# Optimization experiments

Hardware: AMD Instinct MI355X
Metric: run time of the kernel (lower is better)

The kernel has to match this reference:

```python
import jax, jax.numpy as jnp
import numpy as np

B = 256      # graph pairs
NPG = 28     # nodes per graph
MAXN = 32    # max_node_set_size
EPG = 64     # edges per graph (== max_edge_set_size, so no edge padding)
MAXE = 64
D = 128      # node_state_dim
FN = 32      # raw node feature dim
FE = 32      # raw edge feature dim
SK = 64      # sinkhorn_feature_dim
STEPS = 3    # propagation_steps
TEMP = 0.1
ITERS = 20
CW = 0.9     # consistency_weight
G = 2 * B
N = G * NPG
E = G * EPG


def _lin(key, fi, fo):
    return jax.random.normal(key, (fi, fo), jnp.float32) / np.sqrt(fi)


def setup_inputs() -> dict:
    key = jax.random.key(0)
    ks = jax.random.split(key, 12)
    rng = np.random.default_rng(0)
    off = (np.arange(G) * NPG)[:, None]   # graphs ordered q0,c0,q1,c1,...
    from_idx = jnp.asarray((rng.integers(0, NPG, (G, EPG)) + off).reshape(-1), jnp.int32)
    to_idx = jnp.asarray((rng.integers(0, NPG, (G, EPG)) + off).reshape(-1), jnp.int32)
    return dict(
        node_features=jax.random.normal(ks[0], (N, FN), jnp.float32),
        edge_features=jax.random.normal(ks[1], (E, FE), jnp.float32),
        enc_nw=_lin(ks[2], FN, D), enc_nb=jnp.zeros((D,), jnp.float32),
        enc_ew=_lin(ks[3], FE, D), enc_eb=jnp.zeros((D,), jnp.float32),
        msg_w1=_lin(ks[4], 3 * D, 2 * D), msg_b1=jnp.zeros((2 * D,), jnp.float32),
        msg_w2=_lin(ks[5], 2 * D, D), msg_b2=jnp.zeros((D,), jnp.float32),
        rmsg_w1=_lin(ks[6], 3 * D, 2 * D), rmsg_b1=jnp.zeros((2 * D,), jnp.float32),
        rmsg_w2=_lin(ks[7], 2 * D, D), rmsg_b2=jnp.zeros((D,), jnp.float32),
        upd_w1=_lin(ks[8], 2 * D, 2 * D), upd_b1=jnp.zeros((2 * D,), jnp.float32),
        upd_w2=_lin(ks[9], 2 * D, D), upd_b2=jnp.zeros((D,), jnp.float32),
        sk_w1=_lin(ks[10], D, SK), sk_b1=jnp.zeros((SK,), jnp.float32),
        sk_w2=_lin(ks[11], SK, SK), sk_b2=jnp.zeros((SK,), jnp.float32),
        from_idx=from_idx, to_idx=to_idx,
        query_sizes=jnp.full((B,), NPG, jnp.int32),
        corpus_sizes=jnp.full((B,), NPG, jnp.int32),
    )


def _mlp2(x, w1, b1, w2, b2):
    return jnp.maximum(x @ w1 + b1, 0.0) @ w2 + b2


def _sinkhorn(log_alpha):
    # log-domain sinkhorn (noise_factor = 0 -> deterministic)
    la = log_alpha / TEMP
    for _ in range(ITERS):
        la = la - jax.nn.logsumexp(la, axis=2, keepdims=True)
        la = la - jax.nn.logsumexp(la, axis=1, keepdims=True)
    return jnp.exp(la)


def _align(q, c, plan):
    # feature_alignment_score: -relu(q - P @ c).sum over set and feature dims
    return -jnp.maximum(q - plan @ c, 0.0).sum(axis=(1, 2))


def _forward(node_features, edge_features, enc_nw, enc_nb, enc_ew, enc_eb,
             msg_w1, msg_b1, msg_w2, msg_b2, rmsg_w1, rmsg_b1, rmsg_w2, rmsg_b2,
             upd_w1, upd_b1, upd_w2, upd_b2, sk_w1, sk_b1, sk_w2, sk_b2,
             from_idx, to_idx, query_sizes, corpus_sizes):
    h = node_features @ enc_nw + enc_nb        # encoder, [N, D]
    e = edge_features @ enc_ew + enc_eb        # [E, D]

    def messages(h):
        f = _mlp2(jnp.concatenate([h[from_idx], h[to_idx], e], -1), msg_w1, msg_b1, msg_w2, msg_b2)
        r = _mlp2(jnp.concatenate([h[to_idx], h[from_idx], e], -1), rmsg_w1, rmsg_b1, rmsg_w2, rmsg_b2)
        return f, r

    for _ in range(STEPS):  # GraphPropLayer x propagation_steps
        f, r = messages(h)
        agg = jax.ops.segment_sum(f, to_idx, num_segments=N) + \
              jax.ops.segment_sum(r, from_idx, num_segments=N)
        h = h + _mlp2(jnp.concatenate([agg, h], -1), upd_w1, upd_b1, upd_w2, upd_b2)

    # split_and_stack nodes: graphs alternate query/corpus, pad NPG -> MAXN
    hs = jnp.pad(h.reshape(B, 2, NPG, D), ((0, 0), (0, 0), (0, MAXN - NPG), (0, 0)))
    q_nodes, c_nodes = hs[:, 0], hs[:, 1]      # [B, MAXN, D]

    tq = _mlp2(q_nodes, sk_w1, sk_b1, sk_w2, sk_b2)
    tc = _mlp2(c_nodes, sk_w1, sk_b1, sk_w2, sk_b2)
    pos = jnp.arange(MAXN)[None, :]
    mq = tq * (pos < query_sizes[:, None])[..., None]
    mc = tc * (pos < corpus_sizes[:, None])[..., None]
    node_plan = _sinkhorn(jnp.einsum('bqd,bcd->bqc', mq, mc))   # [B, MAXN, MAXN]

    # propagation_messages on final node states
    f, r = messages(h)
    em = (f + r).reshape(B, 2, EPG, D)         # EPG == MAXE -> no pad
    q_edges, c_edges = em[:, 0], em[:, 1]

    # local (within-graph) endpoint indices for kronecker lookup
    fl = (from_idx % NPG).reshape(B, 2, EPG)
    tl = (to_idx % NPG).reshape(B, 2, EPG)
    qf, cf = fl[:, 0], fl[:, 1]
    qt, ct = tl[:, 0], tl[:, 1]

    def kron(T, qf, qt, cf, ct):
        straight = T[qf][:, cf] * T[qt][:, ct]   # [MAXE, MAXE]
        cross = T[qf][:, ct] * T[qt][:, cf]
        return straight + cross

    edge_scores = jax.vmap(kron)(node_plan, qf, qt, cf, ct)     # [B, MAXE, MAXE]
    edge_plan = _sinkhorn(edge_scores)

    return _align(q_nodes, c_nodes, node_plan) + CW * _align(q_edges, c_edges, edge_plan)


def reference(node_features, edge_features, enc_nw, enc_nb, enc_ew, enc_eb,
              msg_w1, msg_b1, msg_w2, msg_b2, rmsg_w1, rmsg_b1, rmsg_w2, rmsg_b2,
              upd_w1, upd_b1, upd_w2, upd_b2, sk_w1, sk_b1, sk_w2, sk_b2,
              from_idx, to_idx, query_sizes, corpus_sizes):
    return _forward(node_features, edge_features, enc_nw, enc_nb, enc_ew, enc_eb,
                    msg_w1, msg_b1, msg_w2, msg_b2, rmsg_w1, rmsg_b1, rmsg_w2, rmsg_b2,
                    upd_w1, upd_b1, upd_w2, upd_b2, sk_w1, sk_b1, sk_w2, sk_b2,
                    from_idx, to_idx, query_sizes, corpus_sizes)
```

## Files before the change

### kernel.cpp

```cpp
#include <hip/hip_runtime.h>
#include <math.h>

#define NPG 28
#define EPG 64
#define NB  256
#define NG  512
#define NN  14336
#define NE  32768
#define TEMPINV 10.0f
#define SINK_ITERS 20
#define CW 0.9f

typedef unsigned int uint;
typedef unsigned short ushort;
typedef __attribute__((ext_vector_type(8))) __bf16 bf16x8;
typedef __attribute__((ext_vector_type(4))) float f32x4;

__device__ __forceinline__ ushort f2bf(float x) {
    uint u = __float_as_uint(x);
    u += 0x7fffu + ((u >> 16) & 1u);
    return (ushort)(u >> 16);
}
__device__ __forceinline__ uint f2bf2(float lo, float hi) {
    return (uint)f2bf(lo) | ((uint)f2bf(hi) << 16);
}
__device__ __forceinline__ float bflo(uint w) { return __uint_as_float(w << 16); }
__device__ __forceinline__ float bfhi(uint w) { return __uint_as_float(w & 0xffff0000u); }
__device__ __forceinline__ uint relu_sum_pk(uint w1, uint w2, uint w3) {
    float lo = fmaxf(bflo(w1) + bflo(w2) + bflo(w3), 0.f);
    float hi = fmaxf(bfhi(w1) + bfhi(w2) + bfhi(w3), 0.f);
    return f2bf2(lo, hi);
}
__device__ __forceinline__ f32x4 mfma16(bf16x8 a, bf16x8 b, f32x4 c) {
    return __builtin_amdgcn_mfma_f32_16x16x32_bf16(a, b, c, 0, 0, 0);
}

__global__ __launch_bounds__(512, 4) void gnn_fused(
    float* __restrict__ h,
    const ushort* __restrict__ EC2,
    const ushort* __restrict__ WhpL,
    const ushort* __restrict__ W2fL, const ushort* __restrict__ W2rL,
    const float* __restrict__ b2f, const float* __restrict__ b2r,
    const ushort* __restrict__ UW1T, const float* __restrict__ ub1,
    const ushort* __restrict__ UW2T, const float* __restrict__ ub2,
    const int* __restrict__ from_idx, const int* __restrict__ to_idx,
    float* __restrict__ EM)
{
    __shared__ ushort HPs[NPG * 520];
    __shared__ float acc_s[NPG * 132];
    __shared__ float hs[NPG * 132];
    __shared__ int fl[64], tl[64];
    const int g = blockIdx.x;
    const int tid = threadIdx.x;
    const int w = tid >> 6, lane = tid & 63;
    const int li = lane & 15, quad = lane >> 4;
    const int wm = w >> 1, wn = w & 1;
    ushort* hid = &HPs[0];

    if (tid < 64) {
        fl[tid] = from_idx[g * 64 + tid] - g * NPG;
        tl[tid] = to_idx[g * 64 + tid] - g * NPG;
    }
    for (int u = tid; u < NPG * 128; u += 512)
        hs[(u >> 7) * 132 + (u & 127)] = h[(size_t)g * (NPG * 128) + u];
    __syncthreads();

#pragma unroll 1
    for (int step = 0; step < 3; ++step) {
        uint4 ha[2][4];
#pragma unroll
        for (int mi = 0; mi < 2; ++mi) {
            const int row = mi * 16 + li;
            const int rr = (row < NPG) ? row : 0;
#pragma unroll
            for (int kb = 0; kb < 4; ++kb) {
                const float* src = &hs[rr * 132 + kb * 32 + quad * 8];
                const float4 f0 = *(const float4*)src;
                const float4 f1 = *(const float4*)(src + 4);
                uint4 o;
                o.x = f2bf2(f0.x, f0.y);
                o.y = f2bf2(f0.z, f0.w);
                o.z = f2bf2(f1.x, f1.y);
                o.w = f2bf2(f1.z, f1.w);
                ha[mi][kb] = o;
            }
        }
        for (int u = tid; u < NPG * 132; u += 512) acc_s[u] = 0.f;

        f32x4 acc[4];
#pragma unroll
        for (int j = 0; j < 4; ++j) acc[j] = f32x4{0.f, 0.f, 0.f, 0.f};

#pragma unroll 1
        for (int p = 0; p < 2; ++p) {
            {
                const int colw = w * 64;
#pragma unroll
                for (int ni = 0; ni < 4; ++ni) {
                    const int col = colw + ni * 16 + li;
                    const ushort* pb = WhpL + (size_t)(p * 512 + col) * 32 + quad * 8;
                    f32x4 c0 = f32x4{0.f, 0.f, 0.f, 0.f};
                    f32x4 c1 = f32x4{0.f, 0.f, 0.f, 0.f};
#pragma unroll
                    for (int kb = 0; kb < 4; ++kb) {
                        const bf16x8 b = __builtin_bit_cast(bf16x8,
                            *(const uint4*)(pb + (size_t)kb * 32768));
                        c0 = mfma16(__builtin_bit_cast(bf16x8, ha[0][kb]), b, c0);
                        c1 = mfma16(__builtin_bit_cast(bf16x8, ha[1][kb]), b, c1);
                    }
#pragma unroll
                    for (int r = 0; r < 4; ++r) {
                        const int r0 = quad * 4 + r;
                        HPs[r0 * 520 + col] = f2bf(c0[r]);
                        const int r1 = 16 + quad * 4 + r;
                        if (r1 < NPG) HPs[r1 * 520 + col] = f2bf(c1[r]);
                    }
                }
            }
            __syncthreads();
            if (p == 1) {
#pragma unroll
                for (int j = 0; j < 4; ++j) acc[j] = f32x4{0.f, 0.f, 0.f, 0.f};
            }
            const int e = wm * 16 + li;
            const int i1 = p ? tl[e] : fl[e];
            const int i2 = p ? fl[e] : tl[e];
            const int ad1 = i1 * 520 + quad * 8;
            const int ad2 = i2 * 520 + 256 + quad * 8;
            const int ade = e * 32 + quad * 8;
            const ushort* ecb = EC2 + (size_t)(g * 2 + p) * 16384;
            const ushort* W2L = p ? W2rL : W2fL;
            const int n0 = wn * 64;
            const ushort* pb[4];
#pragma unroll
            for (int ni = 0; ni < 4; ++ni)
                pb[ni] = W2L + (size_t)(n0 + ni * 16 + li) * 32 + quad * 8;
#pragma unroll
            for (int kb = 0; kb < 8; ++kb) {
                const uint4 u1 = *(const uint4*)&HPs[ad1 + kb * 32];
                const uint4 u2 = *(const uint4*)&HPs[ad2 + kb * 32];
                const uint4 ue = *(const uint4*)(ecb + kb * 2048 + ade);
                uint4 o;
                o.x = relu_sum_pk(u1.x, u2.x, ue.x);
                o.y = relu_sum_pk(u1.y, u2.y, ue.y);
                o.z = relu_sum_pk(u1.z, u2.z, ue.z);
                o.w = relu_sum_pk(u1.w, u2.w, ue.w);
                const bf16x8 a = __builtin_bit_cast(bf16x8, o);
#pragma unroll
                for (int ni = 0; ni < 4; ++ni) {
                    const bf16x8 b = __builtin_bit_cast(bf16x8,
                        *(const uint4*)(pb[ni] + (size_t)kb * 4096));
                    acc[ni] = mfma16(a, b, acc[ni]);
                }
            }
            {
                const int* targ = p ? fl : tl;
                const float* bias = p ? b2r : b2f;
                float bv[4];
#pragma unroll
                for (int ni = 0; ni < 4; ++ni) bv[ni] = bias[n0 + ni * 16 + li];
#pragma unroll
                for (int r = 0; r < 4; ++r) {
                    const int loc = targ[wm * 16 + quad * 4 + r];
#pragma unroll
                    for (int ni = 0; ni < 4; ++ni)
                        atomicAdd(&acc_s[loc * 132 + n0 + ni * 16 + li],
                                  acc[ni][r] + bv[ni]);
                }
            }
            __syncthreads();
        }

        {
            const int n0u = w * 32;
            f32x4 ua[2][2];
#pragma unroll
            for (int mi = 0; mi < 2; ++mi)
#pragma unroll
                for (int ni = 0; ni < 2; ++ni) ua[mi][ni] = f32x4{0.f, 0.f, 0.f, 0.f};
            const ushort* pb0 = UW1T + (size_t)(n0u + li) * 256 + quad * 8;
            const ushort* pb1 = UW1T + (size_t)(n0u + 16 + li) * 256 + quad * 8;
#pragma unroll
            for (int kb = 0; kb < 8; ++kb) {
                bf16x8 a[2];
                if (kb < 4) {
#pragma unroll
                    for (int mi = 0; mi < 2; ++mi) {
                        const int row = mi * 16 + li;
                        const int rr = (row < NPG) ? row : 0;
                        const float* src = &acc_s[rr * 132 + kb * 32 + quad * 8];
                        const float4 f0 = *(const float4*)src;
                        const float4 f1 = *(const float4*)(src + 4);
                        uint4 o;
                        o.x = f2bf2(f0.x, f0.y);
                        o.y = f2bf2(f0.z, f0.w);
                        o.z = f2bf2(f1.x, f1.y);
                        o.w = f2bf2(f1.z, f1.w);
                        a[mi] = __builtin_bit_cast(bf16x8, o);
                    }
                } else {
                    a[0] = __builtin_bit_cast(bf16x8, ha[0][kb - 4]);
                    a[1] = __builtin_bit_cast(bf16x8, ha[1][kb - 4]);
                }
                const bf16x8 b0 = __builtin_bit_cast(bf16x8, *(const uint4*)(pb0 + kb * 32));
                const bf16x8 b1 = __builtin_bit_cast(bf16x8, *(const uint4*)(pb1 + kb * 32));
#pragma unroll
                for (int mi = 0; mi < 2; ++mi) {
                    ua[mi][0] = mfma16(a[mi], b0, ua[mi][0]);
                    ua[mi][1] = mfma16(a[mi], b1, ua[mi][1]);
                }
            }
            const float bv0 = ub1[n0u + li], bv1 = ub1[n0u + 16 + li];
#pragma unroll
            for (int mi = 0; mi < 2; ++mi)
#pragma unroll
                for (int r = 0; r < 4; ++r) {
                    const int row = mi * 16 + quad * 4 + r;
                    if (row < NPG) {
                        hid[row * 264 + n0u + li] = f2bf(fmaxf(ua[mi][0][r] + bv0, 0.f));
                        hid[row * 264 + n0u + 16 + li] = f2bf(fmaxf(ua[mi][1][r] + bv1, 0.f));
                    }
                }
        }
        __syncthreads();
        {
            const int n0u = w * 16;
            f32x4 ua[2];
            ua[0] = f32x4{0.f, 0.f, 0.f, 0.f};
            ua[1] = f32x4{0.f, 0.f, 0.f, 0.f};
            const ushort* pb0 = UW2T + (size_t)(n0u + li) * 256 + quad * 8;
#pragma unroll
            for (int kb = 0; kb < 8; ++kb) {
                bf16x8 a[2];
#pragma unroll
                for (int mi = 0; mi < 2; ++mi) {
                    const int row = mi * 16 + li;
                    const int rr = (row < NPG) ? row : 0;
                    a[mi] = __builtin_bit_cast(bf16x8,
                        *(const uint4*)&hid[rr * 264 + kb * 32 + quad * 8]);
                }
                const bf16x8 b0 = __builtin_bit_cast(bf16x8, *(const uint4*)(pb0 + kb * 32));
                ua[0] = mfma16(a[0], b0, ua[0]);
                ua[1] = mfma16(a[1], b0, ua[1]);
            }
            const float bv = ub2[n0u + li];
#pragma unroll
            for (int mi = 0; mi < 2; ++mi)
#pragma unroll
                for (int r = 0; r < 4; ++r) {
                    const int row = mi * 16 + quad * 4 + r;
                    if (row < NPG)
                        hs[row * 132 + n0u + li] += ua[mi][r] + bv;
                }
        }
        __syncthreads();
    }

    {
        uint4 ha[2][4];
#pragma unroll
        for (int mi = 0; mi < 2; ++mi) {
            const int row = mi * 16 + li;
            const int rr = (row < NPG) ? row : 0;
#pragma unroll
            for (int kb = 0; kb < 4; ++kb) {
                const float* src = &hs[rr * 132 + kb * 32 + quad * 8];
                const float4 f0 = *(const float4*)src;
                const float4 f1 = *(const float4*)(src + 4);
                uint4 o;
                o.x = f2bf2(f0.x, f0.y);
                o.y = f2bf2(f0.z, f0.w);
                o.z = f2bf2(f1.x, f1.y);
                o.w = f2bf2(f1.z, f1.w);
                ha[mi][kb] = o;
            }
        }
        f32x4 acc[4];
#pragma unroll
        for (int j = 0; j < 4; ++j) acc[j] = f32x4{0.f, 0.f, 0.f, 0.f};
        const int n0 = wn * 64;
#pragma unroll 1
        for (int p = 0; p < 2; ++p) {
            {
                const int colw = w * 64;
#pragma unroll
                for (int ni = 0; ni < 4; ++ni) {
                    const int col = colw + ni * 16 + li;
                    const ushort* pb = WhpL + (size_t)(p * 512 + col) * 32 + quad * 8;
                    f32x4 c0 = f32x4{0.f, 0.f, 0.f, 0.f};
                    f32x4 c1 = f32x4{0.f, 0.f, 0.f, 0.f};
#pragma unroll
                    for (int kb = 0; kb < 4; ++kb) {
                        const bf16x8 b = __builtin_bit_cast(bf16x8,
                            *(const uint4*)(pb + (size_t)kb * 32768));
                        c0 = mfma16(__builtin_bit_cast(bf16x8, ha[0][kb]), b, c0);
                        c1 = mfma16(__builtin_bit_cast(bf16x8, ha[1][kb]), b, c1);
                    }
#pragma unroll
                    for (int r = 0; r < 4; ++r) {
                        const int r0 = quad * 4 + r;
                        HPs[r0 * 520 + col] = f2bf(c0[r]);
                        const int r1 = 16 + quad * 4 + r;
                        if (r1 < NPG) HPs[r1 * 520 + col] = f2bf(c1[r]);
                    }
                }
            }
            __syncthreads();
            const int e = wm * 16 + li;
            const int i1 = p ? tl[e] : fl[e];
            const int i2 = p ? fl[e] : tl[e];
            const int ad1 = i1 * 520 + quad * 8;
            const int ad2 = i2 * 520 + 256 + quad * 8;
            const int ade = e * 32 + quad * 8;
            const ushort* ecb = EC2 + (size_t)(g * 2 + p) * 16384;
            const ushort* W2L = p ? W2rL : W2fL;
            const ushort* pb[4];
#pragma unroll
            for (int ni = 0; ni < 4; ++ni)
                pb[ni] = W2L + (size_t)(n0 + ni * 16 + li) * 32 + quad * 8;
#pragma unroll
            for (int kb = 0; kb < 8; ++kb) {
                const uint4 u1 = *(const uint4*)&HPs[ad1 + kb * 32];
                const uint4 u2 = *(const uint4*)&HPs[ad2 + kb * 32];
                const uint4 ue = *(const uint4*)(ecb + kb * 2048 + ade);
                uint4 o;
                o.x = relu_sum_pk(u1.x, u2.x, ue.x);
                o.y = relu_sum_pk(u1.y, u2.y, ue.y);
                o.z = relu_sum_pk(u1.z, u2.z, ue.z);
                o.w = relu_sum_pk(u1.w, u2.w, ue.w);
                const bf16x8 a = __builtin_bit_cast(bf16x8, o);
#pragma unroll
                for (int ni = 0; ni < 4; ++ni) {
                    const bf16x8 b = __builtin_bit_cast(bf16x8,
                        *(const uint4*)(pb[ni] + (size_t)kb * 4096));
                    acc[ni] = mfma16(a, b, acc[ni]);
                }
            }
            __syncthreads();
        }
        float bv[4];
#pragma unroll
        for (int ni = 0; ni < 4; ++ni)
            bv[ni] = b2f[n0 + ni * 16 + li] + b2r[n0 + ni * 16 + li];
#pragma unroll
        for (int r = 0; r < 4; ++r) {
            const int erow = g * 64 + wm * 16 + quad * 4 + r;
#pragma unroll
            for (int ni = 0; ni < 4; ++ni)
                EM[(size_t)erow * 128 + n0 + ni * 16 + li] = acc[ni][r] + bv[ni];
        }
    }
    for (int u = tid; u < NPG * 128; u += 512)
        h[(size_t)g * (NPG * 128) + u] = hs[(u >> 7) * 132 + (u & 127)];
}

template<int TM, bool OUTBF, bool OUT2, bool ECL>
__global__ __launch_bounds__(256) void gemm2(
    const float* __restrict__ A, int lda, int K,
    const float* __restrict__ W, int ldw, const float* __restrict__ bias,
    float* __restrict__ C, ushort* __restrict__ Cb, int ldc)
{
    constexpr int BM = TM * 16;
    constexpr int AV = BM / 64;
    __shared__ float As[16][BM + 4];
    __shared__ float Bs[16][132];
    const int tid = threadIdx.x;
    const int m0 = blockIdx.x * BM;
    const int n0 = blockIdx.y * 128;
    const int tx = tid & 15, ty = tid >> 4;
    const int arow = (AV == 2) ? (tid >> 1) : (tid >> 2);
    const int a0   = (AV == 2) ? ((tid & 1) * 8) : ((tid & 3) * 4);
    const int brow = ty;
    const int bcol = tx * 8;
    const int nch = K >> 4;

    float4 aC[2], bC[2], aN[2], bN[2];
    float acc[TM][8];
#pragma unroll
    for (int i = 0; i < TM; ++i)
#pragma unroll
        for (int j = 0; j < 8; ++j) acc[i][j] = 0.f;

    {
        const float* src = A + (size_t)(m0 + arow) * lda + a0;
        aC[0] = *(const float4*)src;
        if (AV == 2) aC[1] = *(const float4*)(src + 4);
        const float* bsrc = W + (size_t)brow * ldw + n0 + bcol;
        bC[0] = *(const float4*)bsrc;
        bC[1] = *(const float4*)(bsrc + 4);
    }

    for (int ch = 0; ch < nch; ++ch) {
        {
            const float* f = (const float*)aC;
#pragma unroll
            for (int i = 0; i < AV * 4; ++i) As[a0 + i][arow] = f[i];
            *(float4*)&Bs[brow][bcol]     = bC[0];
            *(float4*)&Bs[brow][bcol + 4] = bC[1];
        }
        __syncthreads();
        if (ch + 1 < nch) {
            const int kc = (ch + 1) << 4;
            const float* src = A + (size_t)(m0 + arow) * lda + kc + a0;
            aN[0] = *(const float4*)src;
            if (AV == 2) aN[1] = *(const float4*)(src + 4);
            const float* bsrc = W + (size_t)(kc + brow) * ldw + n0 + bcol;
            bN[0] = *(const float4*)bsrc;
            bN[1] = *(const float4*)(bsrc + 4);
        }
#pragma unroll
        for (int kk = 0; kk < 16; ++kk) {
            float afr[TM], bfr[8];
#pragma unroll
            for (int i = 0; i < TM; i += 4)
                *(float4*)&afr[i] = *(const float4*)&As[kk][ty * TM + i];
            *(float4*)&bfr[0] = *(const float4*)&Bs[kk][tx * 8];
            *(float4*)&bfr[4] = *(const float4*)&Bs[kk][tx * 8 + 4];
#pragma unroll
            for (int i = 0; i < TM; ++i)
#pragma unroll
                for (int j = 0; j < 8; ++j) acc[i][j] = fmaf(afr[i], bfr[j], acc[i][j]);
        }
        __syncthreads();
        aC[0] = aN[0]; aC[1] = aN[1];
        bC[0] = bN[0]; bC[1] = bN[1];
    }
#pragma unroll
    for (int i = 0; i < TM; ++i) {
        const int row = m0 + ty * TM + i;
#pragma unroll
        for (int j = 0; j < 8; ++j) {
            const int col = n0 + tx * 8 + j;
            float v = acc[i][j] + bias[col];
            if (ECL) {
                const int gg = row >> 6, eloc = row & 63;
                const int p = col >> 8, kb = (col >> 5) & 7, jj = col & 31;
                Cb[(size_t)(((gg * 2 + p) * 8 + kb)) * 2048 + eloc * 32 + jj] = f2bf(v);
            } else if (OUTBF) {
                Cb[(size_t)row * ldc + col] = f2bf(v);
            } else {
                C[(size_t)row * ldc + col] = v;
                if (OUT2) Cb[(size_t)row * ldc + col] = f2bf(v);
            }
        }
    }
}

__global__ __launch_bounds__(256) void pack2(
    const float* __restrict__ msg_w1, const float* __restrict__ rmsg_w1,
    const float* __restrict__ msg_b1, const float* __restrict__ rmsg_b1,
    const float* __restrict__ enc_ew, const float* __restrict__ enc_eb,
    const float* __restrict__ msg_w2, const float* __restrict__ rmsg_w2,
    const float* __restrict__ upd_w1, const float* __restrict__ upd_w2,
    float* __restrict__ Wcomb, float* __restrict__ bcomb,
    ushort* __restrict__ WhpL, ushort* __restrict__ W2fL, ushort* __restrict__ W2rL,
    ushort* __restrict__ UW1T, ushort* __restrict__ UW2T)
{
    const int gid = blockIdx.x, tid = threadIdx.x;
    if (gid < 64) {
        const int idx = gid * 256 + tid;
        const int a = idx >> 9, n = idx & 511;
        const float* Wsrc = (n < 256) ? msg_w1 : rmsg_w1;
        const int nc = n & 255;
        float s = 0.f;
        for (int j = 0; j < 128; ++j)
            s = fmaf(enc_ew[a * 128 + j], Wsrc[(256 + j) * 256 + nc], s);
        Wcomb[idx] = s;
    } else if (gid < 66) {
        const int n = (gid - 64) * 256 + tid;
        const float* Wsrc = (n < 256) ? msg_w1 : rmsg_w1;
        const float* bsrc = (n < 256) ? msg_b1 : rmsg_b1;
        const int nc = n & 255;
        float s = bsrc[nc];
        for (int j = 0; j < 128; ++j)
            s = fmaf(enc_eb[j], Wsrc[(256 + j) * 256 + nc], s);
        bcomb[n] = s;
    } else if (gid < 578) {
        const int idx = (gid - 66) * 256 + tid;
        const int n = idx >> 7, k = idx & 127;
        const float* Wsrc = (n < 512) ? msg_w1 : rmsg_w1;
        const int part = (n >> 8) & 1, col = n & 255;
        WhpL[(size_t)(k >> 5) * 32768 + n * 32 + (k & 31)] =
            f2bf(Wsrc[(part * 128 + k) * 256 + col]);
    } else if (gid < 706) {
        const int idx = (gid - 578) * 256 + tid;
        const int n = idx >> 8, k = idx & 255;
        W2fL[(size_t)(k >> 5) * 4096 + n * 32 + (k & 31)] = f2bf(msg_w2[k * 128 + n]);
    } else if (gid < 834) {
        const int idx = (gid - 706) * 256 + tid;
        const int n = idx >> 8, k = idx & 255;
        W2rL[(size_t)(k >> 5) * 4096 + n * 32 + (k & 31)] = f2bf(rmsg_w2[k * 128 + n]);
    } else if (gid < 1090) {
        const int idx = (gid - 834) * 256 + tid;
        const int n = idx >> 8, k = idx & 255;
        UW1T[idx] = f2bf(upd_w1[k * 256 + n]);
    } else {
        const int idx = (gid - 1090) * 256 + tid;
        const int n = idx >> 8, k = idx & 255;
        UW2T[idx] = f2bf(upd_w2[k * 128 + n]);
    }
}

__global__ __launch_bounds__(256) void node_kernel(
    const float* __restrict__ h,
    const float* __restrict__ w1, const float* __restrict__ b1,
    const float* __restrict__ w2, const float* __restrict__ b2,
    const int* __restrict__ qsz, const int* __restrict__ csz,
    float* __restrict__ plan_out, float* __restrict__ loss_out)
{
    __shared__ float qn[32][128];
    __shared__ float cn[32][128];
    __shared__ float t1[32][64];
    __shared__ float mq[32][68];
    __shared__ float mc[32][68];
    __shared__ float la[32][33];
    __shared__ float red[4];
    const int bb = blockIdx.x;
    const int tid = threadIdx.x;
    const int qs = qsz[bb], cs = csz[bb];
    for (int u = tid * 4; u < 4096; u += 1024) {
        const int p = u >> 7, d = u & 127;
        float4 zq = make_float4(0.f, 0.f, 0.f, 0.f), zc = zq;
        if (p < NPG) {
            zq = *(const float4*)(h + (size_t)((2 * bb) * NPG + p) * 128 + d);
            zc = *(const float4*)(h + (size_t)((2 * bb + 1) * NPG + p) * 128 + d);
        }
        *(float4*)&qn[p][d] = zq;
        *(float4*)&cn[p][d] = zc;
    }
    __syncthreads();
    const int col = tid & 63;
    const int rg  = tid >> 6;
    for (int s = 0; s < 2; ++s) {
        const float (*src)[128] = s ? cn : qn;
        float (*dst)[68] = s ? mc : mq;
        const int sz = s ? cs : qs;
        float a8[8];
#pragma unroll
        for (int u = 0; u < 8; ++u) a8[u] = b1[col];
        for (int k = 0; k < 128; ++k) {
            const float wv = w1[k * 64 + col];
#pragma unroll
            for (int u = 0; u < 8; ++u) a8[u] = fmaf(src[rg + 4 * u][k], wv, a8[u]);
        }
#pragma unroll
        for (int u = 0; u < 8; ++u) t1[rg + 4 * u][col] = fmaxf(a8[u], 0.f);
        __syncthreads();
#pragma unroll
        for (int u = 0; u < 8; ++u) a8[u] = b2[col];
        for (int k = 0; k < 64; ++k) {
            const float wv = w2[k * 64 + col];
#pragma unroll
            for (int u = 0; u < 8; ++u) a8[u] = fmaf(t1[rg + 4 * u][k], wv, a8[u]);
        }
#pragma unroll
        for (int u = 0; u < 8; ++u) {
            const int r = rg + 4 * u;
            dst[r][col] = (r < sz) ? a8[u] : 0.f;
        }
        __syncthreads();
    }
    {
        const int q = tid >> 3, cg = tid & 7;
#pragma unroll
        for (int u = 0; u < 4; ++u) {
            const int c = cg + 8 * u;
            float s = 0.f;
            for (int d = 0; d < 64; ++d) s = fmaf(mq[q][d], mc[c][d], s);
            la[q][c] = s * TEMPINV;
        }
    }
    __syncthreads();
    const int l8 = tid & 7, rq = tid >> 3;
    for (int it = 0; it < SINK_ITERS; ++it) {
        {
            float x[4];
#pragma unroll
            for (int u = 0; u < 4; ++u) x[u] = la[rq][l8 * 4 + u];
            float m = fmaxf(fmaxf(x[0], x[1]), fmaxf(x[2], x[3]));
            m = fmaxf(m, __shfl_xor(m, 1));
            m = fmaxf(m, __shfl_xor(m, 2));
            m = fmaxf(m, __shfl_xor(m, 4));
            float s = __expf(x[0] - m) + __expf(x[1] - m) + __expf(x[2] - m) + __expf(x[3] - m);
            s += __shfl_xor(s, 1);
            s += __shfl_xor(s, 2);
            s += __shfl_xor(s, 4);
            const float lse = m + __logf(s);
#pragma unroll
            for (int u = 0; u < 4; ++u) la[rq][l8 * 4 + u] = x[u] - lse;
        }
        __syncthreads();
        {
            float x[4];
#pragma unroll
            for (int u = 0; u < 4; ++u) x[u] = la[l8 * 4 + u][rq];
            float m = fmaxf(fmaxf(x[0], x[1]), fmaxf(x[2], x[3]));
            m = fmaxf(m, __shfl_xor(m, 1));
            m = fmaxf(m, __shfl_xor(m, 2));
            m = fmaxf(m, __shfl_xor(m, 4));
            float s = __expf(x[0] - m) + __expf(x[1] - m) + __expf(x[2] - m) + __expf(x[3] - m);
            s += __shfl_xor(s, 1);
            s += __shfl_xor(s, 2);
            s += __shfl_xor(s, 4);
            const float lse = m + __logf(s);
#pragma unroll
            for (int u = 0; u < 4; ++u) la[l8 * 4 + u][rq] = x[u] - lse;
        }
        __syncthreads();
    }
    for (int u = tid; u < 1024; u += 256) {
        const int q = u >> 5, c = u & 31;
        const float p = __expf(la[q][c]);
        la[q][c] = p;
        plan_out[(size_t)bb * 1024 + u] = p;
    }
    __syncthreads();
    float lsum = 0.f;
    {
        const int q = tid >> 3, dg = tid & 7;
        for (int u = 0; u < 16; ++u) {
            const int d = dg + 8 * u;
            float pc = 0.f;
#pragma unroll
            for (int c = 0; c < 32; ++c) pc = fmaf(la[q][c], cn[c][d], pc);
            lsum += fmaxf(qn[q][d] - pc, 0.f);
        }
    }
#pragma unroll
    for (int off = 1; off < 64; off <<= 1) lsum += __shfl_xor(lsum, off);
    if ((tid & 63) == 0) red[tid >> 6] = lsum;
    __syncthreads();
    if (tid == 0) loss_out[bb] = -(red[0] + red[1] + red[2] + red[3]);
}

__global__ __launch_bounds__(256) void edge_kernel(
    const float* __restrict__ plan, const float* __restrict__ EM,
    const int* __restrict__ from_idx, const int* __restrict__ to_idx,
    float* __restrict__ loss_out)
{
    __shared__ float T[32][33];
    __shared__ float la[64][65];
    __shared__ float ce[64][128];
    __shared__ int qf[64], qt[64], cfi[64], cti[64];
    __shared__ float red[4];
    const int bb = blockIdx.x;
    const int tid = threadIdx.x;
    for (int u = tid; u < 1024; u += 256) T[u >> 5][u & 31] = plan[(size_t)bb * 1024 + u];
    if (tid < 64) {
        const int gq = 2 * bb, gc = 2 * bb + 1;
        qf[tid]  = from_idx[gq * 64 + tid] - gq * NPG;
        qt[tid]  = to_idx  [gq * 64 + tid] - gq * NPG;
        cfi[tid] = from_idx[gc * 64 + tid] - gc * NPG;
        cti[tid] = to_idx  [gc * 64 + tid] - gc * NPG;
    }
    {
        const int gc = 2 * bb + 1;
        for (int u = tid * 4; u < 8192; u += 1024) {
            const int i = u >> 7, d = u & 127;
            *(float4*)&ce[i][d] = *(const float4*)(EM + (size_t)(gc * 64 + i) * 128 + d);
        }
    }
    __syncthreads();
    {
        const int i = tid >> 2, jg = tid & 3;
        const int a = qf[i], b_ = qt[i];
#pragma unroll
        for (int u = 0; u < 16; ++u) {
            const int j = jg * 16 + u;
            const float s = T[a][cfi[j]] * T[b_][cti[j]] + T[a][cti[j]] * T[b_][cfi[j]];
            la[i][j] = s * TEMPINV;
        }
    }
    __syncthreads();
    const int l4 = tid & 3, rr = tid >> 2;
    for (int it = 0; it < SINK_ITERS; ++it) {
        {
            float x[16];
#pragma unroll
            for (int u = 0; u < 16; ++u) x[u] = la[rr][l4 * 16 + u];
            float m = x[0];
#pragma unroll
            for (int u = 1; u < 16; ++u) m = fmaxf(m, x[u]);
            m = fmaxf(m, __shfl_xor(m, 1));
            m = fmaxf(m, __shfl_xor(m, 2));
            float s = 0.f;
#pragma unroll
            for (int u = 0; u < 16; ++u) s += __expf(x[u] - m);
            s += __shfl_xor(s, 1);
            s += __shfl_xor(s, 2);
            const float lse = m + __logf(s);
#pragma unroll
            for (int u = 0; u < 16; ++u) la[rr][l4 * 16 + u] = x[u] - lse;
        }
        __syncthreads();
        {
            float x[16];
#pragma unroll
            for (int u = 0; u < 16; ++u) x[u] = la[l4 * 16 + u][rr];
            float m = x[0];
#pragma unroll
            for (int u = 1; u < 16; ++u) m = fmaxf(m, x[u]);
            m = fmaxf(m, __shfl_xor(m, 1));
            m = fmaxf(m, __shfl_xor(m, 2));
            float s = 0.f;
#pragma unroll
            for (int u = 0; u < 16; ++u) s += __expf(x[u] - m);
            s += __shfl_xor(s, 1);
            s += __shfl_xor(s, 2);
            const float lse = m + __logf(s);
#pragma unroll
            for (int u = 0; u < 16; ++u) la[l4 * 16 + u][rr] = x[u] - lse;
        }
        __syncthreads();
    }
    for (int u = tid; u < 4096; u += 256) la[u >> 6][u & 63] = __expf(la[u >> 6][u & 63]);
    __syncthreads();
    float lsum = 0.f;
    {
        const int q = tid >> 2, dg = tid & 3;
        const float* qe = EM + (size_t)((2 * bb) * 64 + q) * 128;
        for (int u = 0; u < 32; ++u) {
            const int d = dg + 4 * u;
            float pc = 0.f;
            for (int c = 0; c < 64; ++c) pc = fmaf(la[q][c], ce[c][d], pc);
            lsum += fmaxf(qe[d] - pc, 0.f);
        }
    }
#pragma unroll
    for (int off = 1; off < 64; off <<= 1) lsum += __shfl_xor(lsum, off);
    if ((tid & 63) == 0) red[tid >> 6] = lsum;
    __syncthreads();
    if (tid == 0) loss_out[bb] -= CW * (red[0] + red[1] + red[2] + red[3]);
}

extern "C" void kernel_launch(void* const* d_in, const int* in_sizes, int n_in,
                              void* d_out, int out_size, void* d_ws, size_t ws_size,
                              hipStream_t stream)
{
    const float* node_features = (const float*)d_in[0];
    const float* edge_features = (const float*)d_in[1];
    const float* enc_nw  = (const float*)d_in[2];
    const float* enc_nb  = (const float*)d_in[3];
    const float* enc_ew  = (const float*)d_in[4];
    const float* enc_eb  = (const float*)d_in[5];
    const float* msg_w1  = (const float*)d_in[6];
    const float* msg_b1  = (const float*)d_in[7];
    const float* msg_w2  = (const float*)d_in[8];
    const float* msg_b2  = (const float*)d_in[9];
    const float* rmsg_w1 = (const float*)d_in[10];
    const float* rmsg_b1 = (const float*)d_in[11];
    const float* rmsg_w2 = (const float*)d_in[12];
    const float* rmsg_b2 = (const float*)d_in[13];
    const float* upd_w1  = (const float*)d_in[14];
    const float* upd_b1  = (const float*)d_in[15];
    const float* upd_w2  = (const float*)d_in[16];
    const float* upd_b2  = (const float*)d_in[17];
    const float* sk_w1   = (const float*)d_in[18];
    const float* sk_b1   = (const float*)d_in[19];
    const float* sk_w2   = (const float*)d_in[20];
    const float* sk_b2   = (const float*)d_in[21];
    const int* from_idx  = (const int*)d_in[22];
    const int* to_idx    = (const int*)d_in[23];
    const int* qsizes    = (const int*)d_in[24];
    const int* csizes    = (const int*)d_in[25];
    float* out = (float*)d_out;

    float* ws    = (float*)d_ws;
    float* h     = ws;
    float* EM    = h + (size_t)NN * 128;
    float* plan  = EM + (size_t)NE * 128;
    float* Wcomb = plan + (size_t)NB * 1024;
    float* bcomb = Wcomb + 16384;
    ushort* EC2  = (ushort*)(bcomb + 512);
    ushort* WhpL = EC2 + (size_t)NE * 512;
    ushort* W2fL = WhpL + 131072;
    ushort* W2rL = W2fL + 32768;
    ushort* UW1T = W2rL + 32768;
    ushort* UW2T = UW1T + 65536;

    const dim3 blk(256);
    const dim3 blk512(512);

    pack2<<<1218, blk, 0, stream>>>(msg_w1, rmsg_w1, msg_b1, rmsg_b1,
                                    enc_ew, enc_eb, msg_w2, rmsg_w2, upd_w1, upd_w2,
                                    Wcomb, bcomb, WhpL, W2fL, W2rL, UW1T, UW2T);
    gemm2<4, false, false, false><<<dim3(NN / 64, 1), blk, 0, stream>>>(
        node_features, 32, 32, enc_nw, 128, enc_nb, h, nullptr, 128);
    gemm2<8, false, false, true><<<dim3(NE / 128, 4), blk, 0, stream>>>(
        edge_features, 32, 32, Wcomb, 512, bcomb, nullptr, EC2, 512);

    gnn_fused<<<dim3(NG), blk512, 0, stream>>>(
        h, EC2, WhpL, W2fL, W2rL, msg_b2, rmsg_b2,
        UW1T, upd_b1, UW2T, upd_b2, from_idx, to_idx, EM);

    node_kernel<<<NB, blk, 0, stream>>>(
        h, sk_w1, sk_b1, sk_w2, sk_b2, qsizes, csizes, plan, out);
    edge_kernel<<<NB, blk, 0, stream>>>(
        plan, EM, from_idx, to_idx, out);
}
```

Measured before the change: 553.7 us.

## Process two graphs per block in fused GNN kernel to reuse weight fragments

```diff
diff --git a/kernel.cpp b/kernel.cpp
--- a/kernel.cpp
+++ b/kernel.cpp
@@ -35,7 +35,7 @@
     return __builtin_amdgcn_mfma_f32_16x16x32_bf16(a, b, c, 0, 0, 0);
 }
 
-__global__ __launch_bounds__(512, 4) void gnn_fused(
+__global__ __launch_bounds__(512, 2) void gnn_fused(
     float* __restrict__ h,
     const ushort* __restrict__ EC2,
     const ushort* __restrict__ WhpL,
@@ -46,50 +46,52 @@
     const int* __restrict__ from_idx, const int* __restrict__ to_idx,
     float* __restrict__ EM)
 {
-    __shared__ ushort HPs[NPG * 520];
-    __shared__ float acc_s[NPG * 132];
-    __shared__ float hs[NPG * 132];
-    __shared__ int fl[64], tl[64];
+    __shared__ ushort HPs[2][NPG * 520];
+    __shared__ float acc_s[2][NPG * 132];
+    __shared__ float hs[2][NPG * 132];
+    __shared__ int fl[2][64], tl[2][64];
     const int g = blockIdx.x;
     const int tid = threadIdx.x;
     const int w = tid >> 6, lane = tid & 63;
     const int li = lane & 15, quad = lane >> 4;
     const int wm = w >> 1, wn = w & 1;
-    ushort* hid = &HPs[0];
-
-    if (tid < 64) {
-        fl[tid] = from_idx[g * 64 + tid] - g * NPG;
-        tl[tid] = to_idx[g * 64 + tid] - g * NPG;
-    }
-    for (int u = tid; u < NPG * 128; u += 512)
-        hs[(u >> 7) * 132 + (u & 127)] = h[(size_t)g * (NPG * 128) + u];
+
+    if (tid < 128) {
+        const int gr = tid >> 6, e = tid & 63;
+        fl[gr][e] = from_idx[(2 * g + gr) * 64 + e] - (2 * g + gr) * NPG;
+        tl[gr][e] = to_idx[(2 * g + gr) * 64 + e] - (2 * g + gr) * NPG;
+    }
+    for (int u = tid; u < 2 * NPG * 128; u += 512) {
+        const int gr = u / (NPG * 128), v = u % (NPG * 128);
+        hs[gr][(v >> 7) * 132 + (v & 127)] =
+            h[((size_t)(2 * g) * NPG * 128) + (size_t)gr * NPG * 128 + v];
+    }
     __syncthreads();
 
 #pragma unroll 1
     for (int step = 0; step < 3; ++step) {
-        uint4 ha[2][4];
-#pragma unroll
-        for (int mi = 0; mi < 2; ++mi) {
-            const int row = mi * 16 + li;
-            const int rr = (row < NPG) ? row : 0;
-#pragma unroll
-            for (int kb = 0; kb < 4; ++kb) {
-                const float* src = &hs[rr * 132 + kb * 32 + quad * 8];
-                const float4 f0 = *(const float4*)src;
-                const float4 f1 = *(const float4*)(src + 4);
-                uint4 o;
-                o.x = f2bf2(f0.x, f0.y);
-                o.y = f2bf2(f0.z, f0.w);
-                o.z = f2bf2(f1.x, f1.y);
-                o.w = f2bf2(f1.z, f1.w);
-                ha[mi][kb] = o;
-            }
-        }
-        for (int u = tid; u < NPG * 132; u += 512) acc_s[u] = 0.f;
-
-        f32x4 acc[4];
-#pragma unroll
-        for (int j = 0; j < 4; ++j) acc[j] = f32x4{0.f, 0.f, 0.f, 0.f};
+        uint4 ha[2][2][4];
+#pragma unroll
+        for (int gr = 0; gr < 2; ++gr)
+#pragma unroll
+            for (int mi = 0; mi < 2; ++mi) {
+                const int row = mi * 16 + li;
+                const int rr = (row < NPG) ? row : 0;
+#pragma unroll
+                for (int kb = 0; kb < 4; ++kb) {
+                    const float* src = &hs[gr][rr * 132 + kb * 32 + quad * 8];
+                    const float4 f0 = *(const float4*)src;
+                    const float4 f1 = *(const float4*)(src + 4);
+                    uint4 o;
+                    o.x = f2bf2(f0.x, f0.y);
+                    o.y = f2bf2(f0.z, f0.w);
+                    o.z = f2bf2(f1.x, f1.y);
+                    o.w = f2bf2(f1.z, f1.w);
+                    ha[gr][mi][kb] = o;
+                }
+            }
+        for (int u = tid; u < 2 * NPG * 132; u += 512)
+            acc_s[u / (NPG * 132)][u % (NPG * 132)] = 0.f;
 
 #pragma unroll 1
         for (int p = 0; p < 2; ++p) {
@@ -99,186 +101,229 @@
                 for (int ni = 0; ni < 4; ++ni) {
                     const int col = colw + ni * 16 + li;
                     const ushort* pb = WhpL + (size_t)(p * 512 + col) * 32 + quad * 8;
-                    f32x4 c0 = f32x4{0.f, 0.f, 0.f, 0.f};
-                    f32x4 c1 = f32x4{0.f, 0.f, 0.f, 0.f};
+                    f32x4 c[2][2];
+#pragma unroll
+                    for (int gr = 0; gr < 2; ++gr)
+#pragma unroll
+                        for (int mi = 0; mi < 2; ++mi) c[gr][mi] = f32x4{0.f, 0.f, 0.f, 0.f};
 #pragma unroll
                     for (int kb = 0; kb < 4; ++kb) {
                         const bf16x8 b = __builtin_bit_cast(bf16x8,
                             *(const uint4*)(pb + (size_t)kb * 32768));
-                        c0 = mfma16(__builtin_bit_cast(bf16x8, ha[0][kb]), b, c0);
-                        c1 = mfma16(__builtin_bit_cast(bf16x8, ha[1][kb]), b, c1);
+#pragma unroll
+                        for (int gr = 0; gr < 2; ++gr) {
+                            c[gr][0] = mfma16(__builtin_bit_cast(bf16x8, ha[gr][0][kb]), b, c[gr][0]);
+                            c[gr][1] = mfma16(__builtin_bit_cast(bf16x8, ha[gr][1][kb]), b, c[gr][1]);
+                        }
                     }
 #pragma unroll
+                    for (int gr = 0; gr < 2; ++gr)
+#pragma unroll
+                        for (int r = 0; r < 4; ++r) {
+                            const int r0 = quad * 4 + r;
+                            HPs[gr][r0 * 520 + col] = f2bf(c[gr][0][r]);
+                            const int r1 = 16 + quad * 4 + r;
+                            if (r1 < NPG) HPs[gr][r1 * 520 + col] = f2bf(c[gr][1][r]);
+                        }
+                }
+            }
+            __syncthreads();
+
+            const int e = wm * 16 + li;
+            const int n0 = wn * 64;
+            int ad1[2], ad2[2];
+            const ushort* ecb[2];
+#pragma unroll
+            for (int gr = 0; gr < 2; ++gr) {
+                const int i1 = p ? tl[gr][e] : fl[gr][e];
+                const int i2 = p ? fl[gr][e] : tl[gr][e];
+                ad1[gr] = i1 * 520 + quad * 8;
+                ad2[gr] = i2 * 520 + 256 + quad * 8;
+                ecb[gr] = EC2 + (size_t)((2 * g + gr) * 2 + p) * 16384 + e * 32 + quad * 8;
+            }
+            const ushort* W2L = p ? W2rL : W2fL;
+            const ushort* pb[4];
+#pragma unroll
+            for (int ni = 0; ni < 4; ++ni)
+                pb[ni] = W2L + (size_t)(n0 + ni * 16 + li) * 32 + quad * 8;
+
+            f32x4 acc[2][4];
+#pragma unroll
+            for (int gr = 0; gr < 2; ++gr)
+#pragma unroll
+                for (int j = 0; j < 4; ++j) acc[gr][j] = f32x4{0.f, 0.f, 0.f, 0.f};
+#pragma unroll
+            for (int kb = 0; kb < 8; ++kb) {
+                bf16x8 b[4];
+#pragma unroll
+                for (int ni = 0; ni < 4; ++ni)
+                    b[ni] = __builtin_bit_cast(bf16x8,
+                        *(const uint4*)(pb[ni] + (size_t)kb * 4096));
+#pragma unroll
+                for (int gr = 0; gr < 2; ++gr) {
+                    const uint4 u1 = *(const uint4*)&HPs[gr][ad1[gr] + kb * 32];
+                    const uint4 u2 = *(const uint4*)&HPs[gr][ad2[gr] + kb * 32];
+                    const uint4 ue = *(const uint4*)(ecb[gr] + kb * 2048);
+                    uint4 o;
+                    o.x = relu_sum_pk(u1.x, u2.x, ue.x);
+                    o.y = relu_sum_pk(u1.y, u2.y, ue.y);
+                    o.z = relu_sum_pk(u1.z, u2.z, ue.z);
+                    o.w = relu_sum_pk(u1.w, u2.w, ue.w);
+                    const bf16x8 a = __builtin_bit_cast(bf16x8, o);
+#pragma unroll
+                    for (int ni = 0; ni < 4; ++ni)
+                        acc[gr][ni] = mfma16(a, b[ni], acc[gr][ni]);
+                }
+            }
+            {
+                const float* bias = p ? b2r : b2f;
+                float bv[4];
+#pragma unroll
+                for (int ni = 0; ni < 4; ++ni) bv[ni] = bias[n0 + ni * 16 + li];
+#pragma unroll
+                for (int gr = 0; gr < 2; ++gr) {
+                    const int* targ = p ? fl[gr] : tl[gr];
+#pragma unroll
                     for (int r = 0; r < 4; ++r) {
-                        const int r0 = quad * 4 + r;
-                        HPs[r0 * 520 + col] = f2bf(c0[r]);
-                        const int r1 = 16 + quad * 4 + r;
-                        if (r1 < NPG) HPs[r1 * 520 + col] = f2bf(c1[r]);
+                        const int loc = targ[wm * 16 + quad * 4 + r];
+#pragma unroll
+                        for (int ni = 0; ni < 4; ++ni)
+                            atomicAdd(&acc_s[gr][loc * 132 + n0 + ni * 16 + li],
+                                      acc[gr][ni][r] + bv[ni]);
                     }
                 }
             }
             __syncthreads();
-            if (p == 1) {
-#pragma unroll
-                for (int j = 0; j < 4; ++j) acc[j] = f32x4{0.f, 0.f, 0.f, 0.f};
-            }
-            const int e = wm * 16 + li;
-            const int i1 = p ? tl[e] : fl[e];
-            const int i2 = p ? fl[e] : tl[e];
-            const int ad1 = i1 * 520 + quad * 8;
-            const int ad2 = i2 * 520 + 256 + quad * 8;
-            const int ade = e * 32 + quad * 8;
-            const ushort* ecb = EC2 + (size_t)(g * 2 + p) * 16384;
-            const ushort* W2L = p ? W2rL : W2fL;
-            const int n0 = wn * 64;
-            const ushort* pb[4];
-#pragma unroll
-            for (int ni = 0; ni < 4; ++ni)
-                pb[ni] = W2L + (size_t)(n0 + ni * 16 + li) * 32 + quad * 8;
-#pragma unroll
-            for (int kb = 0; kb < 8; ++kb) {
-                const uint4 u1 = *(const uint4*)&HPs[ad1 + kb * 32];
-                const uint4 u2 = *(const uint4*)&HPs[ad2 + kb * 32];
-                const uint4 ue = *(const uint4*)(ecb + kb * 2048 + ade);
-                uint4 o;
-                o.x = relu_sum_pk(u1.x, u2.x, ue.x);
-                o.y = relu_sum_pk(u1.y, u2.y, ue.y);
-                o.z = relu_sum_pk(u1.z, u2.z, ue.z);
-                o.w = relu_sum_pk(u1.w, u2.w, ue.w);
-                const bf16x8 a = __builtin_bit_cast(bf16x8, o);
-#pragma unroll
-                for (int ni = 0; ni < 4; ++ni) {
-                    const bf16x8 b = __builtin_bit_cast(bf16x8,
-                        *(const uint4*)(pb[ni] + (size_t)kb * 4096));
-                    acc[ni] = mfma16(a, b, acc[ni]);
-                }
-            }
-            {
-                const int* targ = p ? fl : tl;
-                const float* bias = p ? b2r : b2f;
-                float bv[4];
-#pragma unroll
-                for (int ni = 0; ni < 4; ++ni) bv[ni] = bias[n0 + ni * 16 + li];
-#pragma unroll
-                for (int r = 0; r < 4; ++r) {
-                    const int loc = targ[wm * 16 + quad * 4 + r];
-#pragma unroll
-                    for (int ni = 0; ni < 4; ++ni)
-                        atomicAdd(&acc_s[loc * 132 + n0 + ni * 16 + li],
-                                  acc[ni][r] + bv[ni]);
-                }
-            }
-            __syncthreads();
         }
 
         {
             const int n0u = w * 32;
-            f32x4 ua[2][2];
-#pragma unroll
-            for (int mi = 0; mi < 2; ++mi)
-#pragma unroll
-                for (int ni = 0; ni < 2; ++ni) ua[mi][ni] = f32x4{0.f, 0.f, 0.f, 0.f};
+            f32x4 ua[2][2][2];
+#pragma unroll
+            for (int gr = 0; gr < 2; ++gr)
+#pragma unroll
+                for (int mi = 0; mi < 2; ++mi)
+#pragma unroll
+                    for (int ni = 0; ni < 2; ++ni) ua[gr][mi][ni] = f32x4{0.f, 0.f, 0.f, 0.f};
             const ushort* pb0 = UW1T + (size_t)(n0u + li) * 256 + quad * 8;
             const ushort* pb1 = UW1T + (size_t)(n0u + 16 + li) * 256 + quad * 8;
 #pragma unroll
             for (int kb = 0; kb < 8; ++kb) {
-                bf16x8 a[2];
-                if (kb < 4) {
+                const bf16x8 b0 = __builtin_bit_cast(bf16x8, *(const uint4*)(pb0 + kb * 32));
+                const bf16x8 b1 = __builtin_bit_cast(bf16x8, *(const uint4*)(pb1 + kb * 32));
+#pragma unroll
+                for (int gr = 0; gr < 2; ++gr) {
+                    bf16x8 a[2];
+                    if (kb < 4) {
+#pragma unroll
+                        for (int mi = 0; mi < 2; ++mi) {
+                            const int row = mi * 16 + li;
+                            const int rr = (row < NPG) ? row : 0;
+                            const float* src = &acc_s[gr][rr * 132 + kb * 32 + quad * 8];
+                            const float4 f0 = *(const float4*)src;
+                            const float4 f1 = *(const float4*)(src + 4);
+                            uint4 o;
+                            o.x = f2bf2(f0.x, f0.y);
+                            o.y = f2bf2(f0.z, f0.w);
+                            o.z = f2bf2(f1.x, f1.y);
+                            o.w = f2bf2(f1.z, f1.w);
+                            a[mi] = __builtin_bit_cast(bf16x8, o);
+                        }
+                    } else {
+                        a[0] = __builtin_bit_cast(bf16x8, ha[gr][0][kb - 4]);
+                        a[1] = __builtin_bit_cast(bf16x8, ha[gr][1][kb - 4]);
+                    }
+#pragma unroll
+                    for (int mi = 0; mi < 2; ++mi) {
+                        ua[gr][mi][0] = mfma16(a[mi], b0, ua[gr][mi][0]);
+                        ua[gr][mi][1] = mfma16(a[mi], b1, ua[gr][mi][1]);
+                    }
+                }
+            }
+            const float bv0 = ub1[n0u + li], bv1 = ub1[n0u + 16 + li];
+#pragma unroll
+            for (int gr = 0; gr < 2; ++gr) {
+                ushort* hid = &HPs[gr][0];
+#pragma unroll
+                for (int mi = 0; mi < 2; ++mi)
+#pragma unroll
+                    for (int r = 0; r < 4; ++r) {
+                        const int row = mi * 16 + quad * 4 + r;
+                        if (row < NPG) {
+                            hid[row * 264 + n0u + li] = f2bf(fmaxf(ua[gr][mi][0][r] + bv0, 0.f));
+                            hid[row * 264 + n0u + 16 + li] = f2bf(fmaxf(ua[gr][mi][1][r] + bv1, 0.f));
+                        }
+                    }
+            }
+        }
+        __syncthreads();
+        {
+            const int n0u = w * 16;
+            f32x4 ua[2][2];
+#pragma unroll
+            for (int gr = 0; gr < 2; ++gr)
+#pragma unroll
+                for (int mi = 0; mi < 2; ++mi) ua[gr][mi] = f32x4{0.f, 0.f, 0.f, 0.f};
+            const ushort* pb0 = UW2T + (size_t)(n0u + li) * 256 + quad * 8;
+#pragma unroll
+            for (int kb = 0; kb < 8; ++kb) {
+                const bf16x8 b0 = __builtin_bit_cast(bf16x8, *(const uint4*)(pb0 + kb * 32));
+#pragma unroll
+                for (int gr = 0; gr < 2; ++gr) {
+                    const ushort* hid = &HPs[gr][0];
 #pragma unroll
                     for (int mi = 0; mi < 2; ++mi) {
                         const int row = mi * 16 + li;
                         const int rr = (row < NPG) ? row : 0;
-                        const float* src = &acc_s[rr * 132 + kb * 32 + quad * 8];
-                        const float4 f0 = *(const float4*)src;
-                        const float4 f1 = *(const float4*)(src + 4);
-                        uint4 o;
-                        o.x = f2bf2(f0.x, f0.y);
-                        o.y = f2bf2(f0.z, f0.w);
-                        o.z = f2bf2(f1.x, f1.y);
-                        o.w = f2bf2(f1.z, f1.w);
-                        a[mi] = __builtin_bit_cast(bf16x8, o);
-                    }
-                } else {
-                    a[0] = __builtin_bit_cast(bf16x8, ha[0][kb - 4]);
-                    a[1] = __builtin_bit_cast(bf16x8, ha[1][kb - 4]);
-                }
-                const bf16x8 b0 = __builtin_bit_cast(bf16x8, *(const uint4*)(pb0 + kb * 32));
-                const bf16x8 b1 = __builtin_bit_cast(bf16x8, *(const uint4*)(pb1 + kb * 32));
-#pragma unroll
-                for (int mi = 0; mi < 2; ++mi) {
-                    ua[mi][0] = mfma16(a[mi], b0, ua[mi][0]);
-                    ua[mi][1] = mfma16(a[mi], b1, ua[mi][1]);
-                }
-            }
-            const float bv0 = ub1[n0u + li], bv1 = ub1[n0u + 16 + li];
-#pragma unroll
-            for (int mi = 0; mi < 2; ++mi)
-#pragma unroll
-                for (int r = 0; r < 4; ++r) {
-                    const int row = mi * 16 + quad * 4 + r;
-                    if (row < NPG) {
-                        hid[row * 264 + n0u + li] = f2bf(fmaxf(ua[mi][0][r] + bv0, 0.f));
-                        hid[row * 264 + n0u + 16 + li] = f2bf(fmaxf(ua[mi][1][r] + bv1, 0.f));
+                        const bf16x8 a = __builtin_bit_cast(bf16x8,
+                            *(const uint4*)&hid[rr * 264 + kb * 32 + quad * 8]);
+                        ua[gr][mi] = mfma16(a, b0, ua[gr][mi]);
                     }
                 }
-        }
-        __syncthreads();
-        {
-            const int n0u = w * 16;
-            f32x4 ua[2];
-            ua[0] = f32x4{0.f, 0.f, 0.f, 0.f};
-            ua[1] = f32x4{0.f, 0.f, 0.f, 0.f};
-            const ushort* pb0 = UW2T + (size_t)(n0u + li) * 256 + quad * 8;
-#pragma unroll
-            for (int kb = 0; kb < 8; ++kb) {
-                bf16x8 a[2];
-#pragma unroll
-                for (int mi = 0; mi < 2; ++mi) {
-                    const int row = mi * 16 + li;
-                    const int rr = (row < NPG) ? row : 0;
-                    a[mi] = __builtin_bit_cast(bf16x8,
-                        *(const uint4*)&hid[rr * 264 + kb * 32 + quad * 8]);
+            }
+            const float bv = ub2[n0u + li];
+#pragma unroll
+            for (int gr = 0; gr < 2; ++gr)
+#pragma unroll
+                for (int mi = 0; mi < 2; ++mi)
+#pragma unroll
+                    for (int r = 0; r < 4; ++r) {
+                        const int row = mi * 16 + quad * 4 + r;
+                        if (row < NPG)
+                            hs[gr][row * 132 + n0u + li] += ua[gr][mi][r] + bv;
+                    }
+        }
+        __syncthreads();
+    }
+
+    {
+        uint4 ha[2][2][4];
+#pragma unroll
+        for (int gr = 0; gr < 2; ++gr)
+#pragma unroll
+            for (int mi = 0; mi < 2; ++mi) {
+                const int row = mi * 16 + li;
+                const int rr = (row < NPG) ? row : 0;
+#pragma unroll
+                for (int kb = 0; kb < 4; ++kb) {
+                    const float* src = &hs[gr][rr * 132 + kb * 32 + quad * 8];
+                    const float4 f0 = *(const float4*)src;
+                    const float4 f1 = *(const float4*)(src + 4);
+                    uint4 o;
+                    o.x = f2bf2(f0.x, f0.y);
+                    o.y = f2bf2(f0.z, f0.w);
+                    o.z = f2bf2(f1.x, f1.y);
+                    o.w = f2bf2(f1.z, f1.w);
+                    ha[gr][mi][kb] = o;
                 }
-                const bf16x8 b0 = __builtin_bit_cast(bf16x8, *(const uint4*)(pb0 + kb * 32));
-                ua[0] = mfma16(a[0], b0, ua[0]);
-                ua[1] = mfma16(a[1], b0, ua[1]);
-            }
-            const float bv = ub2[n0u + li];
-#pragma unroll
-            for (int mi = 0; mi < 2; ++mi)
-#pragma unroll
-                for (int r = 0; r < 4; ++r) {
-                    const int row = mi * 16 + quad * 4 + r;
-                    if (row < NPG)
-                        hs[row * 132 + n0u + li] += ua[mi][r] + bv;
-                }
-        }
-        __syncthreads();
-    }
-
-    {
-        uint4 ha[2][4];
-#pragma unroll
-        for (int mi = 0; mi < 2; ++mi) {
-            const int row = mi * 16 + li;
-            const int rr = (row < NPG) ? row : 0;
-#pragma unroll
-            for (int kb = 0; kb < 4; ++kb) {
-                const float* src = &hs[rr * 132 + kb * 32 + quad * 8];
-                const float4 f0 = *(const float4*)src;
-                const float4 f1 = *(const float4*)(src + 4);
-                uint4 o;
-                o.x = f2bf2(f0.x, f0.y);
-                o.y = f2bf2(f0.z, f0.w);
-                o.z = f2bf2(f1.x, f1.y);
-                o.w = f2bf2(f1.z, f1.w);
-                ha[mi][kb] = o;
-            }
-        }
-        f32x4 acc[4];
-#pragma unroll
-        for (int j = 0; j < 4; ++j) acc[j] = f32x4{0.f, 0.f, 0.f, 0.f};
+            }
+        f32x4 acc[2][4];
+#pragma unroll
+        for (int gr = 0; gr < 2; ++gr)
+#pragma unroll
+            for (int j = 0; j < 4; ++j) acc[gr][j] = f32x4{0.f, 0.f, 0.f, 0.f};
         const int n0 = wn * 64;
+        const int e = wm * 16 + li;
 #pragma unroll 1
         for (int p = 0; p < 2; ++p) {
             {
@@ -287,32 +332,33 @@
                 for (int ni = 0; ni < 4; ++ni) {
                     const int col = colw + ni * 16 + li;
                     const ushort* pb = WhpL + (size_t)(p * 512 + col) * 32 + quad * 8;
-                    f32x4 c0 = f32x4{0.f, 0.f, 0.f, 0.f};
-                    f32x4 c1 = f32x4{0.f, 0.f, 0.f, 0.f};
+                    f32x4 c[2][2];
+#pragma unroll
+                    for (int gr = 0; gr < 2; ++gr)
+#pragma unroll
+                        for (int mi = 0; mi < 2; ++mi) c[gr][mi] = f32x4{0.f, 0.f, 0.f, 0.f};
 #pragma unroll
                     for (int kb = 0; kb < 4; ++kb) {
                         const bf16x8 b = __builtin_bit_cast(bf16x8,
                             *(const uint4*)(pb + (size_t)kb * 32768));
-                        c0 = mfma16(__builtin_bit_cast(bf16x8, ha[0][kb]), b, c0);
-                        c1 = mfma16(__builtin_bit_cast(bf16x8, ha[1][kb]), b, c1);
+#pragma unroll
+                        for (int gr = 0; gr < 2; ++gr) {
+                            c[gr][0] = mfma16(__builtin_bit_cast(bf16x8, ha[gr][0][kb]), b, c[gr][0]);
+                            c[gr][1] = mfma16(__builtin_bit_cast(bf16x8, ha[gr][1][kb]), b, c[gr][1]);
+                        }
                     }
 #pragma unroll
-                    for (int r = 0; r < 4; ++r) {
-                        const int r0 = quad * 4 + r;
-                        HPs[r0 * 520 + col] = f2bf(c0[r]);
-                        const int r1 = 16 + quad * 4 + r;
-                        if (r1 < NPG) HPs[r1 * 520 + col] = f2bf(c1[r]);
-                    }
+                    for (int gr = 0; gr < 2; ++gr)
+#pragma unroll
+                        for (int r = 0; r < 4; ++r) {
+                            const int r0 = quad * 4 + r;
+                            HPs[gr][r0 * 520 + col] = f2bf(c[gr][0][r]);
+                            const int r1 = 16 + quad * 4 + r;
+                            if (r1 < NPG) HPs[gr][r1 * 520 + col] = f2bf(c[gr][1][r]);
+                        }
                 }
             }
             __syncthreads();
-            const int e = wm * 16 + li;
-            const int i1 = p ? tl[e] : fl[e];
-            const int i2 = p ? fl[e] : tl[e];
-            const int ad1 = i1 * 520 + quad * 8;
-            const int ad2 = i2 * 520 + 256 + quad * 8;
-            const int ade = e * 32 + quad * 8;
-            const ushort* ecb = EC2 + (size_t)(g * 2 + p) * 16384;
             const ushort* W2L = p ? W2rL : W2fL;
             const ushort* pb[4];
 #pragma unroll
@@ -320,20 +366,28 @@
                 pb[ni] = W2L + (size_t)(n0 + ni * 16 + li) * 32 + quad * 8;
 #pragma unroll
             for (int kb = 0; kb < 8; ++kb) {
-                const uint4 u1 = *(const uint4*)&HPs[ad1 + kb * 32];
-                const uint4 u2 = *(const uint4*)&HPs[ad2 + kb * 32];
-                const uint4 ue = *(const uint4*)(ecb + kb * 2048 + ade);
-                uint4 o;
-                o.x = relu_sum_pk(u1.x, u2.x, ue.x);
-                o.y = relu_sum_pk(u1.y, u2.y, ue.y);
-                o.z = relu_sum_pk(u1.z, u2.z, ue.z);
-                o.w = relu_sum_pk(u1.w, u2.w, ue.w);
-                const bf16x8 a = __builtin_bit_cast(bf16x8, o);
-#pragma unroll
-                for (int ni = 0; ni < 4; ++ni) {
-                    const bf16x8 b = __builtin_bit_cast(bf16x8,
+                bf16x8 b[4];
+#pragma unroll
+                for (int ni = 0; ni < 4; ++ni)
+                    b[ni] = __builtin_bit_cast(bf16x8,
                         *(const uint4*)(pb[ni] + (size_t)kb * 4096));
-                    acc[ni] = mfma16(a, b, acc[ni]);
+#pragma unroll
+                for (int gr = 0; gr < 2; ++gr) {
+                    const int i1 = p ? tl[gr][e] : fl[gr][e];
+                    const int i2 = p ? fl[gr][e] : tl[gr][e];
+                    const uint4 u1 = *(const uint4*)&HPs[gr][i1 * 520 + quad * 8 + kb * 32];
+                    const uint4 u2 = *(const uint4*)&HPs[gr][i2 * 520 + 256 + quad * 8 + kb * 32];
+                    const uint4 ue = *(const uint4*)(EC2 +
+                        (size_t)((2 * g + gr) * 2 + p) * 16384 + e * 32 + quad * 8 + kb * 2048);
+                    uint4 o;
+                    o.x = relu_sum_pk(u1.x, u2.x, ue.x);
+                    o.y = relu_sum_pk(u1.y, u2.y, ue.y);
+                    o.z = relu_sum_pk(u1.z, u2.z, ue.z);
+                    o.w = relu_sum_pk(u1.w, u2.w, ue.w);
+                    const bf16x8 a = __builtin_bit_cast(bf16x8, o);
+#pragma unroll
+                    for (int ni = 0; ni < 4; ++ni)
+                        acc[gr][ni] = mfma16(a, b[ni], acc[gr][ni]);
                 }
             }
             __syncthreads();
@@ -343,15 +397,20 @@
         for (int ni = 0; ni < 4; ++ni)
             bv[ni] = b2f[n0 + ni * 16 + li] + b2r[n0 + ni * 16 + li];
 #pragma unroll
-        for (int r = 0; r < 4; ++r) {
-            const int erow = g * 64 + wm * 16 + quad * 4 + r;
-#pragma unroll
-            for (int ni = 0; ni < 4; ++ni)
-                EM[(size_t)erow * 128 + n0 + ni * 16 + li] = acc[ni][r] + bv[ni];
-        }
-    }
-    for (int u = tid; u < NPG * 128; u += 512)
-        h[(size_t)g * (NPG * 128) + u] = hs[(u >> 7) * 132 + (u & 127)];
+        for (int gr = 0; gr < 2; ++gr)
+#pragma unroll
+            for (int r = 0; r < 4; ++r) {
+                const int erow = (2 * g + gr) * 64 + wm * 16 + quad * 4 + r;
+#pragma unroll
+                for (int ni = 0; ni < 4; ++ni)
+                    EM[(size_t)erow * 128 + n0 + ni * 16 + li] = acc[gr][ni][r] + bv[ni];
+            }
+    }
+    for (int u = tid; u < 2 * NPG * 128; u += 512) {
+        const int gr = u / (NPG * 128), v = u % (NPG * 128);
+        h[((size_t)(2 * g) * NPG * 128) + (size_t)gr * NPG * 128 + v] =
+            hs[gr][(v >> 7) * 132 + (v & 127)];
+    }
 }
 
 template<int TM, bool OUTBF, bool OUT2, bool ECL>
@@ -789,7 +848,7 @@
     gemm2<8, false, false, true><<<dim3(NE / 128, 4), blk, 0, stream>>>(
         edge_features, 32, 32, Wcomb, 512, bcomb, nullptr, EC2, 512);
 
-    gnn_fused<<<dim3(NG), blk512, 0, stream>>>(
+    gnn_fused<<<dim3(NG / 2), blk512, 0, stream>>>(
         h, EC2, WhpL, W2fL, W2rL, msg_b2, rmsg_b2,
         UW1T, upd_b1, UW2T, upd_b2, from_idx, to_idx, EM);
 
```

After: 540.8 us. -2.3%, faster.
